# Optimization experiments

Hardware: AMD Instinct MI355X
Metric: run time of the kernel (lower is better)

The kernel has to match this reference:

```python
import jax, jax.numpy as jnp
import numpy as np

S, B, N, H = 64, 32, 325, 64

def setup_inputs() -> dict:
    key = jax.random.key(0)
    k1, k2, k3, k4 = jax.random.split(key, 4)
    return {
        "encoder_outputs": jax.random.normal(k1, (S, B, N, H), dtype=jnp.float32),
        "decoder_hidden": jax.random.normal(k2, (B, N, H), dtype=jnp.float32),
        "W": jax.random.normal(k3, (H, H), dtype=jnp.float32) * (1.0 / np.sqrt(H)),
        "b": jax.random.normal(k4, (H,), dtype=jnp.float32) * 0.01,
    }

def reference(encoder_outputs, decoder_hidden, W, b):
    # energy: (S,B,N,H) -- Linear + tanh
    energy = jnp.tanh(jnp.einsum('sbnh,kh->sbnk', encoder_outputs, W) + b)
    # broadcast multiply by decoder_hidden (B,N,H) and reduce over hidden dim -> (S,B,N)
    e = jnp.einsum('sbnh,bnh->sbn', energy, decoder_hidden)
    # softmax over seq_len, output (B,N,S)
    return jax.nn.softmax(jnp.transpose(e, (1, 2, 0)), axis=-1)
```

## Files before the change

### kernel.cpp

```cpp
#include <hip/hip_runtime.h>


constexpr int S = 64, B = 32, N = 325, H = 64;
constexpr int BN = B * N;

__global__ __launch_bounds__(256, 4) void attn_fused(
    const float* __restrict__ enc,
    const float* __restrict__ dec,
    const float* __restrict__ W,
    const float* __restrict__ bias,
    float* __restrict__ out)
{
    const int lane = threadIdx.x & 63;
    const int wave = __builtin_amdgcn_readfirstlane(threadIdx.x >> 6);
    const int bn   = blockIdx.x * 4 + wave;

    const float4* erow = (const float4*)(enc + (lane * BN + bn) * H);
    float4 er[16];
#pragma unroll
    for (int i = 0; i < 16; ++i) er[i] = erow[i];

    const float* drow = dec + bn * H;

    float e_s = 0.0f;
#pragma unroll 2
    for (int k = 0; k < H; ++k) {
        const float4* wrow = (const float4*)(W + k * H);
        float a0 = bias[k], a1 = 0.0f, a2 = 0.0f, a3 = 0.0f;
#pragma unroll
        for (int i = 0; i < 16; ++i) {
            float4 w = wrow[i];
            a0 = fmaf(er[i].x, w.x, a0);
            a1 = fmaf(er[i].y, w.y, a1);
            a2 = fmaf(er[i].z, w.z, a2);
            a3 = fmaf(er[i].w, w.w, a3);
        }
        float a = (a0 + a1) + (a2 + a3);
        float t  = __expf(2.0f * a);
        float th = 1.0f - 2.0f * __builtin_amdgcn_rcpf(t + 1.0f);
        e_s = fmaf(th, drow[k], e_s);
    }

    float m = e_s;
#pragma unroll
    for (int off = 32; off > 0; off >>= 1)
        m = fmaxf(m, __shfl_xor(m, off, 64));
    float p = __expf(e_s - m);
    float sum = p;
#pragma unroll
    for (int off = 32; off > 0; off >>= 1)
        sum += __shfl_xor(sum, off, 64);

    out[bn * S + lane] = p * __builtin_amdgcn_rcpf(sum);
}

extern "C" void kernel_launch(void* const* d_in, const int* in_sizes, int n_in,
                              void* d_out, int out_size, void* d_ws, size_t ws_size,
                              hipStream_t stream) {
    const float* enc  = (const float*)d_in[0];
    const float* dec  = (const float*)d_in[1];
    const float* W    = (const float*)d_in[2];
    const float* bias = (const float*)d_in[3];
    float* out        = (float*)d_out;

    dim3 grid(BN / 4);
    attn_fused<<<grid, 256, 0, stream>>>(enc, dec, W, bias, out);
}
```

Baseline: 315.1 us.

## Chunk hidden dim into four slices accumulating all outputs in registers

```diff
diff --git a/kernel.cpp b/kernel.cpp
--- a/kernel.cpp
+++ b/kernel.cpp
@@ -4,7 +4,9 @@
 constexpr int S = 64, B = 32, N = 325, H = 64;
 constexpr int BN = B * N;
 
-__global__ __launch_bounds__(256, 4) void attn_fused(
+__global__ __launch_bounds__(256)
+__attribute__((amdgpu_waves_per_eu(4, 4)))
+void attn_fused(
     const float* __restrict__ enc,
     const float* __restrict__ dec,
     const float* __restrict__ W,
@@ -15,27 +17,37 @@
     const int wave = __builtin_amdgcn_readfirstlane(threadIdx.x >> 6);
     const int bn   = blockIdx.x * 4 + wave;
 
-    const float4* erow = (const float4*)(enc + (lane * BN + bn) * H);
-    float4 er[16];
-#pragma unroll
-    for (int i = 0; i < 16; ++i) er[i] = erow[i];
-
+    const float* erow = enc + (lane * BN + bn) * H;
     const float* drow = dec + bn * H;
 
+    float acc[64];
+#pragma unroll
+    for (int k = 0; k < 64; ++k) acc[k] = 0.0f;
+
+    for (int hc = 0; hc < 4; ++hc) {
+        const float4* ep = (const float4*)(erow + hc * 16);
+        float4 e0 = ep[0], e1 = ep[1], e2 = ep[2], e3 = ep[3];
+#pragma unroll
+        for (int k = 0; k < 64; ++k) {
+            const float4* wr = (const float4*)(W + k * H + hc * 16);
+            float4 w0 = wr[0], w1 = wr[1], w2 = wr[2], w3 = wr[3];
+            float a = fmaf(e0.x, w0.x, acc[k]);
+            float c = e0.y * w0.y;
+            a = fmaf(e0.z, w0.z, a);   c = fmaf(e0.w, w0.w, c);
+            a = fmaf(e1.x, w1.x, a);   c = fmaf(e1.y, w1.y, c);
+            a = fmaf(e1.z, w1.z, a);   c = fmaf(e1.w, w1.w, c);
+            a = fmaf(e2.x, w2.x, a);   c = fmaf(e2.y, w2.y, c);
+            a = fmaf(e2.z, w2.z, a);   c = fmaf(e2.w, w2.w, c);
+            a = fmaf(e3.x, w3.x, a);   c = fmaf(e3.y, w3.y, c);
+            a = fmaf(e3.z, w3.z, a);   c = fmaf(e3.w, w3.w, c);
+            acc[k] = a + c;
+        }
+    }
+
     float e_s = 0.0f;
-#pragma unroll 2
-    for (int k = 0; k < H; ++k) {
-        const float4* wrow = (const float4*)(W + k * H);
-        float a0 = bias[k], a1 = 0.0f, a2 = 0.0f, a3 = 0.0f;
 #pragma unroll
-        for (int i = 0; i < 16; ++i) {
-            float4 w = wrow[i];
-            a0 = fmaf(er[i].x, w.x, a0);
-            a1 = fmaf(er[i].y, w.y, a1);
-            a2 = fmaf(er[i].z, w.z, a2);
-            a3 = fmaf(er[i].w, w.w, a3);
-        }
-        float a = (a0 + a1) + (a2 + a3);
+    for (int k = 0; k < 64; ++k) {
+        float a  = acc[k] + bias[k];
         float t  = __expf(2.0f * a);
         float th = 1.0f - 2.0f * __builtin_amdgcn_rcpf(t + 1.0f);
         e_s = fmaf(th, drow[k], e_s);
```

New measurement: 324.2 us. 1.03x slower.

## Compute the linear projection with split-bf16 MFMA instead of scalar FMAs

Applied to the files above, without the earlier changes.

```diff
diff --git a/kernel.cpp b/kernel.cpp
--- a/kernel.cpp
+++ b/kernel.cpp
@@ -4,7 +4,24 @@
 constexpr int S = 64, B = 32, N = 325, H = 64;
 constexpr int BN = B * N;
 
-__global__ __launch_bounds__(256, 4) void attn_fused(
+typedef __attribute__((ext_vector_type(8))) short short8;
+typedef __attribute__((ext_vector_type(4))) float f32x4;
+
+union FragU { unsigned u[4]; short8 s8; };
+
+__device__ inline unsigned pack_hi(float x0, float x1, float& r0, float& r1) {
+    unsigned u0 = __builtin_bit_cast(unsigned, x0);
+    unsigned u1 = __builtin_bit_cast(unsigned, x1);
+    r0 = x0 - __builtin_bit_cast(float, u0 & 0xffff0000u);
+    r1 = x1 - __builtin_bit_cast(float, u1 & 0xffff0000u);
+    return (u0 >> 16) | (u1 & 0xffff0000u);
+}
+__device__ inline unsigned pack_bf(float x0, float x1) {
+    return (__builtin_bit_cast(unsigned, x0) >> 16) |
+           (__builtin_bit_cast(unsigned, x1) & 0xffff0000u);
+}
+
+__global__ __launch_bounds__(256) void attn_mfma(
     const float* __restrict__ enc,
     const float* __restrict__ dec,
     const float* __restrict__ W,
@@ -12,33 +29,83 @@
     float* __restrict__ out)
 {
     const int lane = threadIdx.x & 63;
-    const int wave = __builtin_amdgcn_readfirstlane(threadIdx.x >> 6);
-    const int bn   = blockIdx.x * 4 + wave;
+    const int wv   = threadIdx.x >> 6;
+    const int bn   = blockIdx.x * 4 + wv;
+    const int col  = lane & 15;
+    const int grp  = lane >> 4;
 
-    const float4* erow = (const float4*)(enc + (lane * BN + bn) * H);
-    float4 er[16];
+    __shared__ float P[4][16 * 65];
+    float* Pw = P[wv];
+
+    float bias_v[4], dec_v[4];
 #pragma unroll
-    for (int i = 0; i < 16; ++i) er[i] = erow[i];
+    for (int q = 0; q < 4; ++q) {
+        bias_v[q] = bias[q * 16 + col];
+        dec_v[q]  = dec[bn * H + q * 16 + col];
+    }
 
-    const float* drow = dec + bn * H;
+    FragU a_hi[4][2], a_lo[4][2];
+#pragma unroll
+    for (int mt = 0; mt < 4; ++mt) {
+        const float* er = enc + ((mt * 16 + col) * BN + bn) * H;
+#pragma unroll
+        for (int kc = 0; kc < 2; ++kc) {
+            const float4* p4 = (const float4*)(er + kc * 32 + grp * 8);
+            float4 x0 = p4[0], x1 = p4[1];
+            float r0, r1, r2, r3, r4, r5, r6, r7;
+            a_hi[mt][kc].u[0] = pack_hi(x0.x, x0.y, r0, r1);
+            a_hi[mt][kc].u[1] = pack_hi(x0.z, x0.w, r2, r3);
+            a_hi[mt][kc].u[2] = pack_hi(x1.x, x1.y, r4, r5);
+            a_hi[mt][kc].u[3] = pack_hi(x1.z, x1.w, r6, r7);
+            a_lo[mt][kc].u[0] = pack_bf(r0, r1);
+            a_lo[mt][kc].u[1] = pack_bf(r2, r3);
+            a_lo[mt][kc].u[2] = pack_bf(r4, r5);
+            a_lo[mt][kc].u[3] = pack_bf(r6, r7);
+        }
+    }
 
     float e_s = 0.0f;
-#pragma unroll 2
-    for (int k = 0; k < H; ++k) {
-        const float4* wrow = (const float4*)(W + k * H);
-        float a0 = bias[k], a1 = 0.0f, a2 = 0.0f, a3 = 0.0f;
+
+    for (int q = 0; q < 4; ++q) {
+        f32x4 acc[4];
 #pragma unroll
-        for (int i = 0; i < 16; ++i) {
-            float4 w = wrow[i];
-            a0 = fmaf(er[i].x, w.x, a0);
-            a1 = fmaf(er[i].y, w.y, a1);
-            a2 = fmaf(er[i].z, w.z, a2);
-            a3 = fmaf(er[i].w, w.w, a3);
+        for (int mt = 0; mt < 4; ++mt) acc[mt] = (f32x4){0.f, 0.f, 0.f, 0.f};
+
+#pragma unroll
+        for (int kc = 0; kc < 2; ++kc) {
+            const float4* wp = (const float4*)(W + (q * 16 + col) * H + kc * 32 + grp * 8);
+            float4 w0 = wp[0], w1 = wp[1];
+            float r0, r1, r2, r3, r4, r5, r6, r7;
+            FragU b_hi, b_lo;
+            b_hi.u[0] = pack_hi(w0.x, w0.y, r0, r1);
+            b_hi.u[1] = pack_hi(w0.z, w0.w, r2, r3);
+            b_hi.u[2] = pack_hi(w1.x, w1.y, r4, r5);
+            b_hi.u[3] = pack_hi(w1.z, w1.w, r6, r7);
+            b_lo.u[0] = pack_bf(r0, r1);
+            b_lo.u[1] = pack_bf(r2, r3);
+            b_lo.u[2] = pack_bf(r4, r5);
+            b_lo.u[3] = pack_bf(r6, r7);
+#pragma unroll
+            for (int mt = 0; mt < 4; ++mt) {
+                acc[mt] = __builtin_amdgcn_mfma_f32_16x16x32_bf16(a_hi[mt][kc].s8, b_hi.s8, acc[mt], 0, 0, 0);
+                acc[mt] = __builtin_amdgcn_mfma_f32_16x16x32_bf16(a_lo[mt][kc].s8, b_hi.s8, acc[mt], 0, 0, 0);
+                acc[mt] = __builtin_amdgcn_mfma_f32_16x16x32_bf16(a_hi[mt][kc].s8, b_lo.s8, acc[mt], 0, 0, 0);
+            }
         }
-        float a = (a0 + a1) + (a2 + a3);
-        float t  = __expf(2.0f * a);
-        float th = 1.0f - 2.0f * __builtin_amdgcn_rcpf(t + 1.0f);
-        e_s = fmaf(th, drow[k], e_s);
+
+#pragma unroll
+        for (int mt = 0; mt < 4; ++mt) {
+#pragma unroll
+            for (int r = 0; r < 4; ++r) {
+                int s   = mt * 16 + grp * 4 + r;
+                float a = acc[mt][r] + bias_v[q];
+                float t = 1.0f - 2.0f * __builtin_amdgcn_rcpf(__expf(2.0f * a) + 1.0f);
+                Pw[col * 65 + s] = t * dec_v[q];
+            }
+        }
+#pragma unroll
+        for (int k = 0; k < 16; ++k)
+            e_s += Pw[k * 65 + lane];
     }
 
     float m = e_s;
@@ -64,5 +131,5 @@
     float* out        = (float*)d_out;
 
     dim3 grid(BN / 4);
-    attn_fused<<<grid, 256, 0, stream>>>(enc, dec, W, bias, out);
+    attn_mfma<<<grid, 256, 0, stream>>>(enc, dec, W, bias, out);
 }
```

Result: faster. 263.8 us (-16.3%).
